# Kernel tuning notes

Hardware: AMD Instinct MI355X
Metric: run time of the kernel (lower is better)

The kernel has to match this reference:

```python
import jax, jax.numpy as jnp
import numpy as np

N, K, C, D4, HID, HEAD, DEPTH = 40000, 16, 128, 32, 512, 256, 4
EPS = 1e-5  # BatchNorm eps; eval mode with running_mean=0, running_var=1


def _bn(x, g, b):
    # eval-mode BatchNorm1d with fresh running stats (mean=0, var=1)
    return x * (g / np.sqrt(1.0 + EPS)) + b


def _mlp(x, w1, b1, w2, g, b):
    # Linear -> GELU -> Linear(no bias) -> BN
    return _bn(jax.nn.gelu(x @ w1 + b1) @ w2, g, b)


def _lfp(x, lxyz, knn, proj, coor, scale, g, b):
    # LFP: Linear(no bias) -> la_spse_a4 (neighbor gather + anisotropic spatial
    # positional encoding, one PE channel per 4 feature channels, max-pool over k) -> BN
    xp = x @ proj                                   # (N, C)
    xn = xp[knn]                                    # (N, K, C) irregular gather
    rel3 = (lxyz[knn] - lxyz[:, None])[..., :3]     # (N, K, 3)
    pe = jnp.einsum('nkc,cd->nkd', rel3, coor) * jnp.square(scale)  # (N, K, D4)
    out = jnp.max(xn.reshape(N, K, D4, 4) + pe[..., None], axis=1).reshape(N, C)
    return _bn(out, g, b)


def _knn_spse4(lxyz, feat, knn, m_sp, c, h):
    # knn_spse_4: squared anisotropic spatial distances (3 learned 4-d directions
    # per output channel, 12 params) + per-channel color (3) + height (1) weighted
    # squared diffs, averaged over k neighbors; caller takes sqrt.
    rel4 = lxyz[knn] - lxyz[:, None]                # (N, K, 4)
    relf = feat[knn] - feat[:, None]                # (N, K, 4) = color(3)+height(1)
    dirs = m_sp.reshape(3, 4, C)
    e = jnp.zeros((N, K, C), jnp.float32)
    for j in range(3):  # fixed small loop over 3 learned directions
        e = e + jnp.square(jnp.einsum('nkc,cd->nkd', rel4, dirs[j]))
    e = e + jnp.einsum('nki,id->nkd', jnp.square(relf[..., :3]), jnp.square(c))
    e = e + jnp.square(relf[..., 3:4]) * jnp.square(h)
    return jnp.sqrt(e.mean(axis=1))                 # (N, C)


def setup_inputs():
    key = jax.random.key(0)
    ks = jax.random.split(key, 32)
    rn = lambda i, s, sc=0.02: jax.random.normal(ks[i], s, jnp.float32) * sc
    gm = lambda i, s: 1.0 + jax.random.normal(ks[i], s, jnp.float32) * 0.1
    return {
        'x': rn(0, (N, 4), 1.0),
        'xyz': jax.random.uniform(ks[1], (N, 3), jnp.float32),
        'knn': jax.random.randint(ks[2], (N, K), 0, N, jnp.int32),
        'spse_m': rn(3, (12, C), 0.5),
        'spse_c': rn(4, (3, C), 0.5),
        'spse_h': rn(5, (C,), 0.5),
        'nbr_bn0_g': gm(6, (C,)), 'nbr_bn0_b': rn(7, (C,)),
        'nbr_w1': rn(8, (C, 2 * C)), 'nbr_b1': rn(9, (2 * C,)),
        'nbr_w2': rn(10, (2 * C, C)),
        'nbr_bn_g': gm(11, (C,)), 'nbr_bn_b': rn(12, (C,)),
        'lfp_proj': rn(13, (DEPTH, C, C)),
        'lfp_coor': rn(14, (DEPTH, 3, D4), 0.5),
        'lfp_scale': 0.1 + rn(15, (DEPTH, D4), 0.01),
        'lfp_bng': gm(16, (DEPTH, C)), 'lfp_bnb': rn(17, (DEPTH, C)),
        'mlp_w1': rn(18, (3, C, HID)), 'mlp_b1': rn(19, (3, HID)),
        'mlp_w2': rn(20, (3, HID, C)),
        'mlp_bng': gm(21, (3, C)), 'mlp_bnb': rn(22, (3, C)),
        'post_bn_g': gm(23, (C,)), 'post_bn_b': rn(24, (C,)),
        'post_w': rn(25, (C, HEAD)),
    }


def reference(x, xyz, knn, spse_m, spse_c, spse_h, nbr_bn0_g, nbr_bn0_b,
              nbr_w1, nbr_b1, nbr_w2, nbr_bn_g, nbr_bn_b,
              lfp_proj, lfp_coor, lfp_scale, lfp_bng, lfp_bnb,
              mlp_w1, mlp_b1, mlp_w2, mlp_bng, mlp_bnb,
              post_bn_g, post_bn_b, post_w):
    # Stage.forward, first==last stage, eval mode (no drop_path, no closs).
    lxyz = jnp.pad(xyz, ((0, 0), (0, 1)))  # cor_std = 1.0
    nbr = _knn_spse4(lxyz, x, knn, spse_m, spse_c, spse_h)
    nbr = _bn(nbr, nbr_bn0_g, nbr_bn0_b)
    nbr = jax.nn.gelu(nbr @ nbr_w1 + nbr_b1) @ nbr_w2   # nbr_proj
    h = _bn(nbr, nbr_bn_g, nbr_bn_b)                    # nbr_bn; x = nbr (first stage)
    # Block: residual MLP, then DEPTH LFPs with an MLP after every 2nd LFP
    h = h + _mlp(h, mlp_w1[0], mlp_b1[0], mlp_w2[0], mlp_bng[0], mlp_bnb[0])
    for i in range(DEPTH):
        h = h + _lfp(h, lxyz, knn, lfp_proj[i], lfp_coor[i], lfp_scale[i],
                     lfp_bng[i], lfp_bnb[i])
        if i % 2 == 1:
            j = i // 2 + 1
            h = h + _mlp(h, mlp_w1[j], mlp_b1[j], mlp_w2[j], mlp_bng[j], mlp_bnb[j])
    return _bn(h, post_bn_g, post_bn_b) @ post_w        # postproj -> (N, HEAD)
```

## Files before the change

kernel.cpp:

```cpp
#include <hip/hip_runtime.h>
#include <hip/hip_bf16.h>
#include <math.h>

#define NPTS 40000
#define KNB 16
#define CH 128

typedef unsigned short u16;
typedef __attribute__((ext_vector_type(8))) short bf16x8;
typedef __attribute__((ext_vector_type(4))) float f32x4;

__device__ __forceinline__ float gelu_f(float v) {
  const float u = 0.7978845608028654f * (v + 0.044715f * v * v * v);
  const float t = __builtin_amdgcn_exp2f(-2.8853900817779268f * u);
  return v * __builtin_amdgcn_rcpf(1.0f + t);
}

__device__ __forceinline__ float bnscale(float g) {
  return g * rsqrtf(1.0f + 1e-5f);
}

__device__ __forceinline__ u16 f2bf(float x) {
  union { __hip_bfloat16 b; u16 u; } cv;
  cv.b = __float2bfloat16(x);
  return cv.u;
}

__device__ __forceinline__ float bf2f(u16 u) {
  union { float f; unsigned int i; } cv;
  cv.i = ((unsigned int)u) << 16;
  return cv.f;
}

__device__ __forceinline__ void bf16split(float x, u16& hi, u16& lo) {
  hi = f2bf(x);
  lo = f2bf(x - bf2f(hi));
}

__device__ __forceinline__ void gl2lds(const u16* gp, u16* lp) {
  __builtin_amdgcn_global_load_lds(
      (const __attribute__((address_space(1))) void*)gp,
      (__attribute__((address_space(3))) void*)lp, 16, 0, 0);
}

__global__ __launch_bounds__(128) void spse_kernel(
    const float* __restrict__ x, const float* __restrict__ xyz,
    const int* __restrict__ knn, const float* __restrict__ sm,
    const float* __restrict__ sc, const float* __restrict__ sh,
    const float* __restrict__ g0, const float* __restrict__ b0,
    u16* __restrict__ oh, u16* __restrict__ ol) {
  const int n = blockIdx.x;
  const int c = threadIdx.x;
  __shared__ float sr[KNB][3];
  __shared__ float sf[KNB][4];
  if (c < KNB) {
    const int j = knn[n * KNB + c];
    sr[c][0] = xyz[j * 3 + 0] - xyz[n * 3 + 0];
    sr[c][1] = xyz[j * 3 + 1] - xyz[n * 3 + 1];
    sr[c][2] = xyz[j * 3 + 2] - xyz[n * 3 + 2];
    float f0 = x[j * 4 + 0] - x[n * 4 + 0];
    float f1 = x[j * 4 + 1] - x[n * 4 + 1];
    float f2 = x[j * 4 + 2] - x[n * 4 + 2];
    float f3 = x[j * 4 + 3] - x[n * 4 + 3];
    sf[c][0] = f0 * f0; sf[c][1] = f1 * f1;
    sf[c][2] = f2 * f2; sf[c][3] = f3 * f3;
  }
  __syncthreads();
  const float m0 = sm[c], m1 = sm[CH + c], m2 = sm[2 * CH + c];
  const float m4 = sm[4 * CH + c], m5 = sm[5 * CH + c], m6 = sm[6 * CH + c];
  const float m8 = sm[8 * CH + c], m9 = sm[9 * CH + c], m10 = sm[10 * CH + c];
  float c0 = sc[c];          c0 *= c0;
  float c1 = sc[CH + c];     c1 *= c1;
  float c2 = sc[2 * CH + c]; c2 *= c2;
  float h2 = sh[c];          h2 *= h2;
  float e = 0.0f;
#pragma unroll
  for (int k = 0; k < KNB; k++) {
    const float r0 = sr[k][0], r1 = sr[k][1], r2 = sr[k][2];
    const float d0 = fmaf(r2, m2, fmaf(r1, m1, r0 * m0));
    const float d1 = fmaf(r2, m6, fmaf(r1, m5, r0 * m4));
    const float d2 = fmaf(r2, m10, fmaf(r1, m9, r0 * m8));
    e = fmaf(d0, d0, e);
    e = fmaf(d1, d1, e);
    e = fmaf(d2, d2, e);
    e = fmaf(sf[k][0], c0, e);
    e = fmaf(sf[k][1], c1, e);
    e = fmaf(sf[k][2], c2, e);
    e = fmaf(sf[k][3], h2, e);
  }
  const float v = sqrtf(e * (1.0f / KNB)) * bnscale(g0[c]) + b0[c];
  u16 hi, lo; bf16split(v, hi, lo);
  const size_t idx = (size_t)n * CH + c;
  oh[idx] = hi; ol[idx] = lo;
}

__global__ __launch_bounds__(256) void lfp_kernel(
    const u16* __restrict__ xp, const int* __restrict__ knn,
    const float* __restrict__ xyz, const float* __restrict__ coor,
    const float* __restrict__ scale, const float* __restrict__ g,
    const float* __restrict__ b, u16* __restrict__ hh, u16* __restrict__ hl) {
  const int t = threadIdx.x;
  const int bid = blockIdx.x;
  __shared__ int si[16][KNB];
  __shared__ float sr[16][KNB][3];
  {
    const int pp = t >> 4, kk = t & 15;
    const int n = bid * 16 + pp;
    const int j = knn[n * KNB + kk];
    si[pp][kk] = j;
    sr[pp][kk][0] = xyz[j * 3 + 0] - xyz[n * 3 + 0];
    sr[pp][kk][1] = xyz[j * 3 + 1] - xyz[n * 3 + 1];
    sr[pp][kk][2] = xyz[j * 3 + 2] - xyz[n * 3 + 2];
  }
  __syncthreads();
  const int p = t >> 4, d8 = t & 15;
  const int n = bid * 16 + p;
  const float c0a = coor[d8 * 2],     c1a = coor[32 + d8 * 2],     c2a = coor[64 + d8 * 2];
  const float c0b = coor[d8 * 2 + 1], c1b = coor[32 + d8 * 2 + 1], c2b = coor[64 + d8 * 2 + 1];
  float s2a = scale[d8 * 2];     s2a *= s2a;
  float s2b = scale[d8 * 2 + 1]; s2b *= s2b;
  float a[8];
#pragma unroll
  for (int e = 0; e < 8; e++) a[e] = -3.0e38f;
#pragma unroll
  for (int k = 0; k < KNB; k++) {
    const int j = si[p][k];
    const float r0 = sr[p][k][0], r1 = sr[p][k][1], r2 = sr[p][k][2];
    const float pea = fmaf(r2, c2a, fmaf(r1, c1a, r0 * c0a)) * s2a;
    const float peb = fmaf(r2, c2b, fmaf(r1, c1b, r0 * c0b)) * s2b;
    const bf16x8 v = *(const bf16x8*)(xp + (size_t)j * CH + d8 * 8);
#pragma unroll
    for (int e = 0; e < 4; e++) a[e] = fmaxf(a[e], bf2f((u16)v[e]) + pea);
#pragma unroll
    for (int e = 4; e < 8; e++) a[e] = fmaxf(a[e], bf2f((u16)v[e]) + peb);
  }
  const size_t off = (size_t)n * CH + d8 * 8;
  union { u16 a[8]; uint4 v; } ih, il, oh, ol;
  ih.v = *(const uint4*)(hh + off);
  il.v = *(const uint4*)(hl + off);
#pragma unroll
  for (int e = 0; e < 8; e++) {
    const int c = d8 * 8 + e;
    const float nv = bf2f(ih.a[e]) + bf2f(il.a[e]) + a[e] * bnscale(g[c]) + b[c];
    u16 hi, lo; bf16split(nv, hi, lo);
    oh.a[e] = hi; ol.a[e] = lo;
  }
  *(uint4*)(hh + off) = oh.v;
  *(uint4*)(hl + off) = ol.v;
}

__global__ __launch_bounds__(256) void prep_weights(
    const float* __restrict__ nw1, const float* __restrict__ nw2,
    const float* __restrict__ mw1, const float* __restrict__ mw2,
    const float* __restrict__ lproj, const float* __restrict__ pw,
    const float* __restrict__ pg, u16* __restrict__ th, u16* __restrict__ tl) {
  const int idx = blockIdx.x * 256 + threadIdx.x;
  const float* src;
  int local, Kd, Nd, dst, swz;
  float scale = 1.0f;
  if (idx < 32768)        { src = nw1; local = idx;          Kd = 128; Nd = 256; dst = 0; swz = 0; }
  else if (idx < 65536)   { src = nw2; local = idx - 32768;  Kd = 256; Nd = 128; dst = 32768; swz = 1; }
  else if (idx < 262144)  { int j = (idx - 65536) >> 16;  local = (idx - 65536) & 65535;
                            src = mw1 + j * 65536; Kd = 128; Nd = 512; dst = 65536 + j * 65536; swz = 0; }
  else if (idx < 458752)  { int j = (idx - 262144) >> 16; local = (idx - 262144) & 65535;
                            src = mw2 + j * 65536; Kd = 512; Nd = 128; dst = 262144 + j * 65536; swz = 1; }
  else if (idx < 524288)  { int i = (idx - 458752) >> 14; local = (idx - 458752) & 16383;
                            src = lproj + i * 16384; Kd = 128; Nd = 128; dst = 458752 + i * 16384; swz = 0; }
  else if (idx < 557056)  { local = idx - 524288; src = pw; Kd = 128; Nd = 256; dst = 524288; swz = 0;
                            scale = bnscale(pg[local >> 8]); }
  else return;
  const int k = local / Nd, n = local % Nd;
  const float v = src[local] * scale;
  u16 hi, lo; bf16split(v, hi, lo);
  const int ks = swz ? ((k & ~63) | ((k & 63) ^ ((n & 7) << 3))) : k;
  const int o = dst + n * Kd + ks;
  th[o] = hi; tl[o] = lo;
}

__global__ __launch_bounds__(256) void fold_pb(const float* __restrict__ pw,
                                               const float* __restrict__ pb,
                                               float* __restrict__ fb) {
  const int t = threadIdx.x;
  float a = 0.0f;
  for (int k = 0; k < 128; k++) a = fmaf(pb[k], pw[k * 256 + t], a);
  fb[t] = a;
}

template <int EPI, int NSPLIT>
__global__ __launch_bounds__(256, 2) void k128_reg(
    const u16* __restrict__ Ahi, const u16* __restrict__ Alo,
    const u16* __restrict__ Wth, const u16* __restrict__ Wtl,
    const float* __restrict__ p0, u16* __restrict__ outu,
    float* __restrict__ outf, int ostride, int ntiles) {
  const int t = threadIdx.x, lane = t & 63, w = t >> 6;
  const int col0 = blockIdx.y * 128;
  const int wm0 = (w >> 1) * 32, wn0 = (w & 1) * 64;
  const int lc = lane & 15, lq = lane >> 4;
  const int lq8 = lq * 8, lq4 = lq * 4;

  bf16x8 wh[4][4], wl[4][4];
  float bv[4];
#pragma unroll
  for (int nf = 0; nf < 4; nf++) {
    const int nr = col0 + wn0 + nf * 16 + lc;
    const u16* wr = Wth + (size_t)nr * 128;
    const u16* wr2 = Wtl + (size_t)nr * 128;
#pragma unroll
    for (int ks = 0; ks < 4; ks++) {
      wh[nf][ks] = *(const bf16x8*)(wr + ks * 32 + lq8);
      wl[nf][ks] = *(const bf16x8*)(wr2 + ks * 32 + lq8);
    }
    bv[nf] = (EPI == 0) ? 0.0f : p0[nr];
  }

  const f32x4 zz = {0.0f, 0.0f, 0.0f, 0.0f};
  for (int tile = blockIdx.x; tile < ntiles; tile += gridDim.x) {
    const int row0 = tile * 64;
    f32x4 acc[2][4];
#pragma unroll
    for (int mf = 0; mf < 2; mf++)
#pragma unroll
      for (int nf = 0; nf < 4; nf++) acc[mf][nf] = zz;
#pragma unroll
    for (int ks = 0; ks < 4; ks++) {
      bf16x8 ah[2], al[2];
#pragma unroll
      for (int mf = 0; mf < 2; mf++) {
        const size_t ao = (size_t)(row0 + wm0 + mf * 16 + lc) * 128 + ks * 32 + lq8;
        ah[mf] = *(const bf16x8*)(Ahi + ao);
        if (NSPLIT == 3) al[mf] = *(const bf16x8*)(Alo + ao);
      }
#pragma unroll
      for (int mf = 0; mf < 2; mf++)
#pragma unroll
        for (int nf = 0; nf < 4; nf++) {
          acc[mf][nf] = __builtin_amdgcn_mfma_f32_16x16x32_bf16(ah[mf], wh[nf][ks], acc[mf][nf], 0, 0, 0);
          acc[mf][nf] = __builtin_amdgcn_mfma_f32_16x16x32_bf16(ah[mf], wl[nf][ks], acc[mf][nf], 0, 0, 0);
          if (NSPLIT == 3)
            acc[mf][nf] = __builtin_amdgcn_mfma_f32_16x16x32_bf16(al[mf], wh[nf][ks], acc[mf][nf], 0, 0, 0);
        }
    }
#pragma unroll
    for (int mf = 0; mf < 2; mf++)
#pragma unroll
      for (int q = 0; q < 4; q++) {
        const int r = row0 + wm0 + mf * 16 + lq4 + q;
#pragma unroll
        for (int nf = 0; nf < 4; nf++) {
          const int col = col0 + wn0 + nf * 16 + lc;
          const size_t off = (size_t)r * ostride + col;
          const float v = acc[mf][nf][q];
          if (EPI == 0)      outu[off] = f2bf(v);
          else if (EPI == 1) outu[off] = f2bf(gelu_f(v + bv[nf]));
          else               outf[off] = v + bv[nf];
        }
      }
  }
}

template <int K, bool RES>
__global__ __launch_bounds__(256, 3) void gemm_w2(
    const u16* __restrict__ A, const u16* __restrict__ Wth,
    const u16* __restrict__ Wtl, const float* __restrict__ g,
    const float* __restrict__ bb, u16* __restrict__ hh, u16* __restrict__ hl) {
  __shared__ __align__(16) u16 Ws[2][128 * 64];
  const int t = threadIdx.x, lane = t & 63, w = t >> 6;
  const int row0 = blockIdx.x * 64;
  const int wm0 = (w >> 1) * 32, wn0 = (w & 1) * 64;
  const int lc = lane & 15, lq = lane >> 4;
  const int lq8 = lq * 8, lq4 = lq * 4;

  const f32x4 zz = {0.0f, 0.0f, 0.0f, 0.0f};
  f32x4 acc[2][4];
#pragma unroll
  for (int mf = 0; mf < 2; mf++)
#pragma unroll
    for (int nf = 0; nf < 4; nf++) acc[mf][nf] = zz;

  auto stage_slab = [&](u16* lds, int kb) {
#pragma unroll
    for (int i = 0; i < 1024; i += 256) {
      const int wc0 = i + w * 64;
      const int c = wc0 + lane;
      gl2lds(Wth + (size_t)(c >> 3) * K + kb + (c & 7) * 8, lds + wc0 * 8);
    }
  };
  auto load_af = [&](bf16x8 (&dst)[2][2], int kb) {
#pragma unroll
    for (int mf = 0; mf < 2; mf++)
#pragma unroll
      for (int ks = 0; ks < 2; ks++)
        dst[mf][ks] = *(const bf16x8*)(A + (size_t)(row0 + wm0 + mf * 16 + lc) * K +
                                       kb + ks * 32 + lq8);
  };

  bf16x8 afc[2][2], afn[2][2];
  stage_slab(Ws[0], 0);
  load_af(afc, 0);
  __syncthreads();

  constexpr int NT = K / 64;
#pragma unroll 2
  for (int tt = 0; tt < NT; tt++) {
    const int cur = tt & 1;
    if (tt + 1 < NT) {
      stage_slab(Ws[cur ^ 1], (tt + 1) * 64);
      load_af(afn, (tt + 1) * 64);
    }
#pragma unroll
    for (int ks = 0; ks < 2; ks++) {
      bf16x8 whf[4], wlf[4];
#pragma unroll
      for (int nf = 0; nf < 4; nf++) {
        const int nr = wn0 + nf * 16 + lc;
        const int j = (ks * 32 + lq8) ^ ((nr & 7) << 3);
        whf[nf] = *(const bf16x8*)(Ws[cur] + nr * 64 + j);
        wlf[nf] = *(const bf16x8*)(Wtl + (size_t)nr * K + tt * 64 + j);
      }
#pragma unroll
      for (int mf = 0; mf < 2; mf++)
#pragma unroll
        for (int nf = 0; nf < 4; nf++) {
          acc[mf][nf] = __builtin_amdgcn_mfma_f32_16x16x32_bf16(afc[mf][ks], whf[nf], acc[mf][nf], 0, 0, 0);
          acc[mf][nf] = __builtin_amdgcn_mfma_f32_16x16x32_bf16(afc[mf][ks], wlf[nf], acc[mf][nf], 0, 0, 0);
        }
    }
    __syncthreads();
#pragma unroll
    for (int mf = 0; mf < 2; mf++)
#pragma unroll
      for (int ks = 0; ks < 2; ks++) afc[mf][ks] = afn[mf][ks];
  }

  float S0[4], S1[4];
#pragma unroll
  for (int nf = 0; nf < 4; nf++) {
    const int col = wn0 + nf * 16 + lc;
    S0[nf] = bnscale(g[col]);
    S1[nf] = bb[col];
  }
#pragma unroll
  for (int mf = 0; mf < 2; mf++)
#pragma unroll
    for (int q = 0; q < 4; q++) {
      const int r = row0 + wm0 + mf * 16 + lq4 + q;
#pragma unroll
      for (int nf = 0; nf < 4; nf++) {
        const int col = wn0 + nf * 16 + lc;
        const size_t off = (size_t)r * CH + col;
        float v = acc[mf][nf][q] * S0[nf] + S1[nf];
        if (RES) v += bf2f(hh[off]) + bf2f(hl[off]);
        u16 hi, lo; bf16split(v, hi, lo);
        hh[off] = hi; hl[off] = lo;
      }
    }
}

extern "C" void kernel_launch(void* const* d_in, const int* in_sizes, int n_in,
                              void* d_out, int out_size, void* d_ws, size_t ws_size,
                              hipStream_t stream) {
  const float* x    = (const float*)d_in[0];
  const float* xyz  = (const float*)d_in[1];
  const int*   knn  = (const int*)d_in[2];
  const float* sm   = (const float*)d_in[3];
  const float* scc  = (const float*)d_in[4];
  const float* shh  = (const float*)d_in[5];
  const float* bn0g = (const float*)d_in[6];
  const float* bn0b = (const float*)d_in[7];
  const float* nw1  = (const float*)d_in[8];
  const float* nb1  = (const float*)d_in[9];
  const float* nw2  = (const float*)d_in[10];
  const float* nbng = (const float*)d_in[11];
  const float* nbnb = (const float*)d_in[12];
  const float* lproj  = (const float*)d_in[13];
  const float* lcoor  = (const float*)d_in[14];
  const float* lscale = (const float*)d_in[15];
  const float* lbng   = (const float*)d_in[16];
  const float* lbnb   = (const float*)d_in[17];
  const float* mw1  = (const float*)d_in[18];
  const float* mb1  = (const float*)d_in[19];
  const float* mw2  = (const float*)d_in[20];
  const float* mbng = (const float*)d_in[21];
  const float* mbnb = (const float*)d_in[22];
  const float* pg   = (const float*)d_in[23];
  const float* pb   = (const float*)d_in[24];
  const float* pw   = (const float*)d_in[25];
  float* out = (float*)d_out;

  char* ws = (char*)d_ws;
  u16*   h_hi = (u16*)(ws + 0);
  u16*   h_lo = (u16*)(ws + 10240000);
  u16*   act  = (u16*)(ws + 20480000);
  u16*   xp   = (u16*)(ws + 20480000);
  u16*   Wh   = (u16*)(ws + 61440000);
  u16*   Wl   = (u16*)(ws + 62554112);
  float* fb   = (float*)(ws + 63668224);

  const u16* nw1t   = Wh + 0;
  const u16* nw2t   = Wh + 32768;
  const u16* mw1t   = Wh + 65536;
  const u16* mw2t   = Wh + 262144;
  const u16* lprojt = Wh + 458752;
  const u16* postt  = Wh + 524288;
  const u16* nw1tl   = Wl + 0;
  const u16* nw2tl   = Wl + 32768;
  const u16* mw1tl   = Wl + 65536;
  const u16* mw2tl   = Wl + 262144;
  const u16* lprojtl = Wl + 458752;
  const u16* posttl  = Wl + 524288;

  prep_weights<<<2176, 256, 0, stream>>>(nw1, nw2, mw1, mw2, lproj, pw, pg, Wh, Wl);
  fold_pb<<<1, 256, 0, stream>>>(pw, pb, fb);

  spse_kernel<<<NPTS, 128, 0, stream>>>(x, xyz, knn, sm, scc, shh, bn0g, bn0b, h_hi, h_lo);

  k128_reg<1, 2><<<dim3(256, 2), 256, 0, stream>>>(h_hi, h_lo, nw1t, nw1tl, nb1,
                                                   act, nullptr, 256, 625);
  gemm_w2<256, false><<<625, 256, 0, stream>>>(act, nw2t, nw2tl, nbng, nbnb, h_hi, h_lo);

  k128_reg<1, 2><<<dim3(128, 4), 256, 0, stream>>>(h_hi, h_lo, mw1t, mw1tl, mb1,
                                                   act, nullptr, 512, 625);
  gemm_w2<512, true><<<625, 256, 0, stream>>>(act, mw2t, mw2tl, mbng, mbnb, h_hi, h_lo);

  for (int i = 0; i < 4; i++) {
    k128_reg<0, 2><<<dim3(625, 1), 256, 0, stream>>>(h_hi, h_lo, lprojt + i * 16384,
                                                     lprojtl + i * 16384, nullptr,
                                                     xp, nullptr, 128, 625);
    lfp_kernel<<<2500, 256, 0, stream>>>(xp, knn, xyz, lcoor + i * 96, lscale + i * 32,
                                         lbng + i * 128, lbnb + i * 128, h_hi, h_lo);
    if (i & 1) {
      const int j = i / 2 + 1;
      k128_reg<1, 2><<<dim3(128, 4), 256, 0, stream>>>(h_hi, h_lo, mw1t + j * 65536,
                                                       mw1tl + j * 65536, mb1 + j * 512,
                                                       act, nullptr, 512, 625);
      gemm_w2<512, true><<<625, 256, 0, stream>>>(act, mw2t + j * 65536, mw2tl + j * 65536,
                                                  mbng + j * 128, mbnb + j * 128,
                                                  h_hi, h_lo);
    }
  }

  k128_reg<2, 3><<<dim3(256, 2), 256, 0, stream>>>(h_hi, h_lo, postt, posttl, fb,
                                                   nullptr, out, 256, 625);
}
```

Measured before the change: 462.9 us.

## Fuse LFP projection GEMM into epilogues of preceding residual kernels

The standalone LFP projection GEMM (h @ proj) is removed. Each of the four projections is now computed in the epilogue of whichever kernel last wrote h: the MLP second GEMM or the previous LFP kernel. The freshly written hi-part of h is staged in swizzled shared memory and multiplied by the projection weights with MFMA, writing into ping-pong xp buffers. This drops four kernel launches and four re-reads of h, at the cost of more registers and LDS per block and projecting only the hi bf16 part of h.

```diff
diff --git a/kernel.cpp b/kernel.cpp
--- a/kernel.cpp
+++ b/kernel.cpp
@@ -94,15 +94,19 @@
   oh[idx] = hi; ol[idx] = lo;
 }
 
+template <bool XP>
 __global__ __launch_bounds__(256) void lfp_kernel(
     const u16* __restrict__ xp, const int* __restrict__ knn,
     const float* __restrict__ xyz, const float* __restrict__ coor,
     const float* __restrict__ scale, const float* __restrict__ g,
-    const float* __restrict__ b, u16* __restrict__ hh, u16* __restrict__ hl) {
+    const float* __restrict__ b, const u16* __restrict__ pjh,
+    const u16* __restrict__ pjl, u16* __restrict__ xpo,
+    u16* __restrict__ hh, u16* __restrict__ hl) {
   const int t = threadIdx.x;
   const int bid = blockIdx.x;
   __shared__ int si[16][KNB];
   __shared__ float sr[16][KNB][3];
+  __shared__ __align__(16) u16 Hs[16 * 128];
   {
     const int pp = t >> 4, kk = t & 15;
     const int n = bid * 16 + pp;
@@ -147,6 +151,46 @@
   }
   *(uint4*)(hh + off) = oh.v;
   *(uint4*)(hl + off) = ol.v;
+
+  if constexpr (XP) {
+    {
+      const int c0 = d8 * 8;
+      const int cs0 = (c0 & ~63) | ((c0 & 63) ^ ((p & 7) << 3));
+      *(uint4*)(Hs + p * 128 + cs0) = oh.v;
+    }
+    __syncthreads();
+    const int lane = t & 63, w = t >> 6;
+    const int lc = lane & 15, lq = lane >> 4;
+    const int lq8 = lq * 8, lq4 = lq * 4;
+    bf16x8 ph_[2][4], pl_[2][4];
+#pragma unroll
+    for (int nf = 0; nf < 2; nf++)
+#pragma unroll
+      for (int ks = 0; ks < 4; ks++) {
+        const size_t wo = (size_t)(w * 32 + nf * 16 + lc) * 128 + ks * 32 + lq8;
+        ph_[nf][ks] = *(const bf16x8*)(pjh + wo);
+        pl_[nf][ks] = *(const bf16x8*)(pjl + wo);
+      }
+    const f32x4 zz = {0.0f, 0.0f, 0.0f, 0.0f};
+    f32x4 xacc[2] = {zz, zz};
+#pragma unroll
+    for (int ks = 0; ks < 4; ks++) {
+      const int j = ks * 32 + lq8;
+      const int cs = (j & ~63) | ((j & 63) ^ ((lc & 7) << 3));
+      const bf16x8 aF = *(const bf16x8*)(Hs + lc * 128 + cs);
+#pragma unroll
+      for (int nf = 0; nf < 2; nf++) {
+        xacc[nf] = __builtin_amdgcn_mfma_f32_16x16x32_bf16(aF, ph_[nf][ks], xacc[nf], 0, 0, 0);
+        xacc[nf] = __builtin_amdgcn_mfma_f32_16x16x32_bf16(aF, pl_[nf][ks], xacc[nf], 0, 0, 0);
+      }
+    }
+#pragma unroll
+    for (int q = 0; q < 4; q++)
+#pragma unroll
+      for (int nf = 0; nf < 2; nf++)
+        xpo[(size_t)(bid * 16 + lq4 + q) * CH + w * 32 + nf * 16 + lc] =
+            f2bf(xacc[nf][q]);
+  }
 }
 
 __global__ __launch_bounds__(256) void prep_weights(
@@ -210,7 +254,7 @@
       wh[nf][ks] = *(const bf16x8*)(wr + ks * 32 + lq8);
       wl[nf][ks] = *(const bf16x8*)(wr2 + ks * 32 + lq8);
     }
-    bv[nf] = (EPI == 0) ? 0.0f : p0[nr];
+    bv[nf] = p0[nr];
   }
 
   const f32x4 zz = {0.0f, 0.0f, 0.0f, 0.0f};
@@ -250,19 +294,20 @@
           const int col = col0 + wn0 + nf * 16 + lc;
           const size_t off = (size_t)r * ostride + col;
           const float v = acc[mf][nf][q];
-          if (EPI == 0)      outu[off] = f2bf(v);
-          else if (EPI == 1) outu[off] = f2bf(gelu_f(v + bv[nf]));
-          else               outf[off] = v + bv[nf];
+          if (EPI == 1) outu[off] = f2bf(gelu_f(v + bv[nf]));
+          else          outf[off] = v + bv[nf];
         }
       }
   }
 }
 
-template <int K, bool RES>
+template <int K, bool RES, bool XP>
 __global__ __launch_bounds__(256, 3) void gemm_w2(
     const u16* __restrict__ A, const u16* __restrict__ Wth,
     const u16* __restrict__ Wtl, const float* __restrict__ g,
-    const float* __restrict__ bb, u16* __restrict__ hh, u16* __restrict__ hl) {
+    const float* __restrict__ bb, const u16* __restrict__ pjh,
+    const u16* __restrict__ pjl, u16* __restrict__ xpo,
+    u16* __restrict__ hh, u16* __restrict__ hl) {
   __shared__ __align__(16) u16 Ws[2][128 * 64];
   const int t = threadIdx.x, lane = t & 63, w = t >> 6;
   const int row0 = blockIdx.x * 64;
@@ -332,6 +377,7 @@
       for (int ks = 0; ks < 2; ks++) afc[mf][ks] = afn[mf][ks];
   }
 
+  u16* Hs = &Ws[0][0];
   float S0[4], S1[4];
 #pragma unroll
   for (int nf = 0; nf < 4; nf++) {
@@ -352,8 +398,57 @@
         if (RES) v += bf2f(hh[off]) + bf2f(hl[off]);
         u16 hi, lo; bf16split(v, hi, lo);
         hh[off] = hi; hl[off] = lo;
-      }
-    }
+        if constexpr (XP) {
+          const int rl = wm0 + mf * 16 + lq4 + q;
+          const int cs = (col & ~63) | ((col & 63) ^ ((rl & 7) << 3));
+          Hs[rl * 128 + cs] = hi;
+        }
+      }
+    }
+
+  if constexpr (XP) {
+    __syncthreads();
+    bf16x8 ph_[2][4], pl_[2][4];
+#pragma unroll
+    for (int nf = 0; nf < 2; nf++)
+#pragma unroll
+      for (int ks = 0; ks < 4; ks++) {
+        const size_t wo = (size_t)(w * 32 + nf * 16 + lc) * 128 + ks * 32 + lq8;
+        ph_[nf][ks] = *(const bf16x8*)(pjh + wo);
+        pl_[nf][ks] = *(const bf16x8*)(pjl + wo);
+      }
+    f32x4 xacc[4][2];
+#pragma unroll
+    for (int mf = 0; mf < 4; mf++)
+#pragma unroll
+      for (int nf = 0; nf < 2; nf++) xacc[mf][nf] = zz;
+#pragma unroll
+    for (int ks = 0; ks < 4; ks++) {
+      const int j = ks * 32 + lq8;
+      bf16x8 aF[4];
+#pragma unroll
+      for (int mf = 0; mf < 4; mf++) {
+        const int r = mf * 16 + lc;
+        const int cs = (j & ~63) | ((j & 63) ^ ((r & 7) << 3));
+        aF[mf] = *(const bf16x8*)(Hs + r * 128 + cs);
+      }
+#pragma unroll
+      for (int mf = 0; mf < 4; mf++)
+#pragma unroll
+        for (int nf = 0; nf < 2; nf++) {
+          xacc[mf][nf] = __builtin_amdgcn_mfma_f32_16x16x32_bf16(aF[mf], ph_[nf][ks], xacc[mf][nf], 0, 0, 0);
+          xacc[mf][nf] = __builtin_amdgcn_mfma_f32_16x16x32_bf16(aF[mf], pl_[nf][ks], xacc[mf][nf], 0, 0, 0);
+        }
+    }
+#pragma unroll
+    for (int mf = 0; mf < 4; mf++)
+#pragma unroll
+      for (int q = 0; q < 4; q++)
+#pragma unroll
+        for (int nf = 0; nf < 2; nf++)
+          xpo[(size_t)(row0 + mf * 16 + lq4 + q) * CH + w * 32 + nf * 16 + lc] =
+              f2bf(xacc[mf][nf][q]);
+  }
 }
 
 extern "C" void kernel_launch(void* const* d_in, const int* in_sizes, int n_in,
@@ -391,10 +486,11 @@
   u16*   h_hi = (u16*)(ws + 0);
   u16*   h_lo = (u16*)(ws + 10240000);
   u16*   act  = (u16*)(ws + 20480000);
-  u16*   xp   = (u16*)(ws + 20480000);
-  u16*   Wh   = (u16*)(ws + 61440000);
-  u16*   Wl   = (u16*)(ws + 62554112);
-  float* fb   = (float*)(ws + 63668224);
+  u16*   xpA  = (u16*)(ws + 61440000);
+  u16*   xpB  = (u16*)(ws + 71680000);
+  u16*   Wh   = (u16*)(ws + 81920000);
+  u16*   Wl   = (u16*)(ws + 83034112);
+  float* fb   = (float*)(ws + 84148224);
 
   const u16* nw1t   = Wh + 0;
   const u16* nw2t   = Wh + 32768;
@@ -416,28 +512,41 @@
 
   k128_reg<1, 2><<<dim3(256, 2), 256, 0, stream>>>(h_hi, h_lo, nw1t, nw1tl, nb1,
                                                    act, nullptr, 256, 625);
-  gemm_w2<256, false><<<625, 256, 0, stream>>>(act, nw2t, nw2tl, nbng, nbnb, h_hi, h_lo);
+  gemm_w2<256, false, false><<<625, 256, 0, stream>>>(
+      act, nw2t, nw2tl, nbng, nbnb, nullptr, nullptr, nullptr, h_hi, h_lo);
 
   k128_reg<1, 2><<<dim3(128, 4), 256, 0, stream>>>(h_hi, h_lo, mw1t, mw1tl, mb1,
                                                    act, nullptr, 512, 625);
-  gemm_w2<512, true><<<625, 256, 0, stream>>>(act, mw2t, mw2tl, mbng, mbnb, h_hi, h_lo);
-
-  for (int i = 0; i < 4; i++) {
-    k128_reg<0, 2><<<dim3(625, 1), 256, 0, stream>>>(h_hi, h_lo, lprojt + i * 16384,
-                                                     lprojtl + i * 16384, nullptr,
-                                                     xp, nullptr, 128, 625);
-    lfp_kernel<<<2500, 256, 0, stream>>>(xp, knn, xyz, lcoor + i * 96, lscale + i * 32,
-                                         lbng + i * 128, lbnb + i * 128, h_hi, h_lo);
-    if (i & 1) {
-      const int j = i / 2 + 1;
-      k128_reg<1, 2><<<dim3(128, 4), 256, 0, stream>>>(h_hi, h_lo, mw1t + j * 65536,
-                                                       mw1tl + j * 65536, mb1 + j * 512,
-                                                       act, nullptr, 512, 625);
-      gemm_w2<512, true><<<625, 256, 0, stream>>>(act, mw2t + j * 65536, mw2tl + j * 65536,
-                                                  mbng + j * 128, mbnb + j * 128,
-                                                  h_hi, h_lo);
-    }
-  }
+  gemm_w2<512, true, true><<<625, 256, 0, stream>>>(
+      act, mw2t, mw2tl, mbng, mbnb, lprojt, lprojtl, xpA, h_hi, h_lo);
+
+  lfp_kernel<true><<<2500, 256, 0, stream>>>(
+      xpA, knn, xyz, lcoor + 0 * 96, lscale + 0 * 32, lbng + 0 * 128, lbnb + 0 * 128,
+      lprojt + 16384, lprojtl + 16384, xpB, h_hi, h_lo);
+
+  lfp_kernel<false><<<2500, 256, 0, stream>>>(
+      xpB, knn, xyz, lcoor + 1 * 96, lscale + 1 * 32, lbng + 1 * 128, lbnb + 1 * 128,
+      nullptr, nullptr, nullptr, h_hi, h_lo);
+  k128_reg<1, 2><<<dim3(128, 4), 256, 0, stream>>>(h_hi, h_lo, mw1t + 65536,
+                                                   mw1tl + 65536, mb1 + 512,
+                                                   act, nullptr, 512, 625);
+  gemm_w2<512, true, true><<<625, 256, 0, stream>>>(
+      act, mw2t + 65536, mw2tl + 65536, mbng + 128, mbnb + 128,
+      lprojt + 2 * 16384, lprojtl + 2 * 16384, xpA, h_hi, h_lo);
+
+  lfp_kernel<true><<<2500, 256, 0, stream>>>(
+      xpA, knn, xyz, lcoor + 2 * 96, lscale + 2 * 32, lbng + 2 * 128, lbnb + 2 * 128,
+      lprojt + 3 * 16384, lprojtl + 3 * 16384, xpB, h_hi, h_lo);
+
+  lfp_kernel<false><<<2500, 256, 0, stream>>>(
+      xpB, knn, xyz, lcoor + 3 * 96, lscale + 3 * 32, lbng + 3 * 128, lbnb + 3 * 128,
+      nullptr, nullptr, nullptr, h_hi, h_lo);
+  k128_reg<1, 2><<<dim3(128, 4), 256, 0, stream>>>(h_hi, h_lo, mw1t + 2 * 65536,
+                                                   mw1tl + 2 * 65536, mb1 + 2 * 512,
+                                                   act, nullptr, 512, 625);
+  gemm_w2<512, true, false><<<625, 256, 0, stream>>>(
+      act, mw2t + 2 * 65536, mw2tl + 2 * 65536, mbng + 2 * 128, mbnb + 2 * 128,
+      nullptr, nullptr, nullptr, h_hi, h_lo);
 
   k128_reg<2, 3><<<dim3(256, 2), 256, 0, stream>>>(h_hi, h_lo, postt, posttl, fb,
                                                    nullptr, out, 256, 625);
```

After: 425.3 us. 1.09x faster.
